# Kernel optimization log

Hardware: AMD Instinct MI355X
Metric: run time of the kernel (lower is better)

The kernel has to match this reference:

```python
import jax, jax.numpy as jnp
import numpy as np

B, C, T = 16, 768, 9
S = T * T * T            # 729 tokens
H = 8                    # heads
E = 3                    # experts
HID = C * 4              # expert hidden dim (mult=4)


def setup_inputs() -> dict:
    key = jax.random.key(0)
    ks = jax.random.split(key, 8)
    w = lambda k, sh: (jax.random.normal(k, sh, jnp.float32) * 0.02)
    return {
        "x": jax.random.normal(ks[0], (B, C, T, T, T), jnp.float32),
        "ln_gamma": jnp.ones((C, T, T, T), jnp.float32),
        "ln_beta": jnp.zeros((C, T, T, T), jnp.float32),
        "w_qkv": w(ks[1], (C, 3 * C)),
        "w_out": w(ks[2], (C, C)),
        "w_gate": w(ks[3], (C, E)),
        "b_gate": jnp.zeros((E,), jnp.float32),
        "w1": w(ks[4], (E, C, HID)),
        "b1": jnp.zeros((E, HID), jnp.float32),
        "w2": w(ks[5], (E, HID, C)),
        "b2": jnp.zeros((E, C), jnp.float32),
    }


def reference(x, ln_gamma, ln_beta, w_qkv, w_out, w_gate, b_gate, w1, b1, w2, b2):
    b = x.shape[0]
    # LayerNorm over (C, T, H, W) per batch element, affine params [C,T,T,T]
    mu = jnp.mean(x, axis=(1, 2, 3, 4), keepdims=True)
    var = jnp.var(x, axis=(1, 2, 3, 4), keepdims=True)
    xn = (x - mu) * jax.lax.rsqrt(var + 1e-5) * ln_gamma + ln_beta

    # ---- attention (NOTE: source applies no 1/sqrt(d) scaling) ----
    tok = xn.reshape(b, C, S).transpose(0, 2, 1)                 # [b,s,c]
    qkv = (tok @ w_qkv).reshape(b, S, 3, H, C // H)              # [b,s,3,h,d]
    q = qkv[:, :, 0].transpose(0, 2, 1, 3)                       # [b,h,s,d]
    k = qkv[:, :, 1].transpose(0, 2, 1, 3)
    v = qkv[:, :, 2].transpose(0, 2, 1, 3)
    attn = jax.nn.softmax(jnp.einsum('bhqd,bhkd->bhqk', q, k), axis=-1)
    ctx = jnp.einsum('bhqk,bhkd->bqhd', attn, v).reshape(b, S, C)
    attn_out = (ctx @ w_out).transpose(0, 2, 1).reshape(b, C, T, T, T)
    x2 = x + attn_out                                            # residual (dropout = eval identity)

    # ---- switch-MoE (top-1 gate, all experts computed densely then masked) ----
    tok2 = x2.reshape(b, C, S).transpose(0, 2, 1)                # [b,s,c]
    gate = jax.nn.softmax(tok2 @ w_gate + b_gate, axis=-1)       # [b,s,E]
    mask = jax.nn.one_hot(jnp.argmax(gate, axis=-1), E, dtype=gate.dtype)
    mg = gate * mask
    denom = jnp.sum(mg, axis=0, keepdims=True) + 1e-6            # sum over dim 0, per source
    gate_scores = mg / denom * b                                 # capacity = int(1.0 * b)

    hmid = jax.nn.gelu(jnp.einsum('bsc,ech->bseh', tok2, w1) + b1, approximate=False)
    eout = jnp.einsum('bseh,ehc->bsec', hmid, w2) + b2           # [b,s,E,c]
    moe = jnp.einsum('bse,bsec->bsc', gate_scores, eout)         # weighted mix over experts

    out = x2 + moe.transpose(0, 2, 1).reshape(b, C, T, T, T)
    return out
```

## Files before the change

### kernel.cpp

```cpp
#include <hip/hip_runtime.h>

typedef __bf16 bf16;
typedef __bf16 bf16x4_t __attribute__((ext_vector_type(4)));
typedef __bf16 bf16x8_t __attribute__((ext_vector_type(8)));
typedef float f32x4 __attribute__((ext_vector_type(4)));

#define DEVI __device__ __forceinline__

#define N_B   16
#define N_C   768
#define N_S   729
#define N_TOK 11664
#define TOKP  11776
#define N_H   8
#define N_D   96
#define N_HID 3072
#define MOE_TILES 94
#define GATE_BLOCKS 183

#define OFF_WQKVH 0ull
#define OFF_WQKVL 3538944ull
#define OFF_WOUTH 7077888ull
#define OFF_WOUTL 8257536ull
#define OFF_W1T   9437184ull
#define OFF_W2T   23592960ull
#define OFF_XTOK  37748736ull
#define OFF_R3    73924608ull
#define OFF_TOKH  OFF_R3
#define OFF_TOKL  (OFF_R3 + 18087936ull)
#define OFF_VTH   OFF_R3
#define OFF_VTL   (OFF_R3 + 18087936ull)
#define OFF_T2H   OFF_R3
#define OFF_QKH   110100480ull
#define OFF_QKL   146276352ull
#define OFF_VPH   182452224ull
#define OFF_VPL   200540160ull
#define OFF_CTXH  OFF_VPH
#define OFF_CTXL  OFF_VPL
#define OFF_HMID  OFF_QKH
#define OFF_X2    218628096ull
#define OFF_STATS 254803968ull
#define OFF_DENOM (OFF_STATS + 256ull)
#define OFF_SEL   (OFF_STATS + 16384ull)
#define OFF_PVAL  (OFF_SEL + 65536ull)
#define OFF_GSV   (OFF_PVAL + 65536ull)
#define OFF_PERM  (OFF_GSV + 65536ull)
#define OFF_CNT   (OFF_PERM + 65536ull)

DEVI f32x4 mfma16(bf16x8_t a, bf16x8_t b, f32x4 c) {
  return __builtin_amdgcn_mfma_f32_16x16x32_bf16(a, b, c, 0, 0, 0);
}
DEVI bf16 f2bf(float f) { return (bf16)f; }
DEVI float bf2f(bf16 h) { return (float)h; }
#define GLDS(gp, lp) __builtin_amdgcn_global_load_lds( \
    (__attribute__((address_space(1))) void*)(gp),     \
    (__attribute__((address_space(3))) void*)(lp), 16, 0, 0)

DEVI void xcd_swz(int& bx, int& by) {
  int gx = gridDim.x;
  int nwg = gx * gridDim.y;
  int lin = blockIdx.x + gx * blockIdx.y;
  int xcd = lin & 7, j = lin >> 3;
  int q = nwg >> 3, r = nwg & 7;
  int base = (xcd < r) ? xcd * (q + 1) : r * (q + 1) + (xcd - r) * q;
  int g = base + j;
  by = g / gx;
  bx = g - by * gx;
}

template<bool SPLIT>
__global__ void kxpose(const float* __restrict__ in, bf16* __restrict__ oh,
                       bf16* __restrict__ ol, int R, int Cc) {
  __shared__ float T[32][33];
  int c0 = blockIdx.x * 32, r0 = blockIdx.y * 32;
  int tx = threadIdx.x, ty = threadIdx.y;
#pragma unroll
  for (int i = 0; i < 4; i++)
    T[ty + i * 8][tx] = in[(size_t)(r0 + ty + i * 8) * Cc + c0 + tx];
  __syncthreads();
#pragma unroll
  for (int i = 0; i < 4; i++) {
    float v = T[tx][ty + i * 8];
    size_t o = (size_t)(c0 + ty + i * 8) * R + r0 + tx;
    bf16 hh = f2bf(v);
    oh[o] = hh;
    if constexpr (SPLIT) ol[o] = f2bf(v - bf2f(hh));
  }
}

__global__ __launch_bounds__(256) void ln_stats(const float* __restrict__ x,
                                                double* __restrict__ stats) {
  int b = blockIdx.x >> 7, ch = blockIdx.x & 127;
  const float* xb = x + (size_t)b * 559872;
  int start = ch * 4374;
  float s = 0.f, ss = 0.f;
  for (int i = start + threadIdx.x; i < start + 4374; i += 256) {
    float v = xb[i];
    s += v; ss += v * v;
  }
#pragma unroll
  for (int o = 32; o > 0; o >>= 1) { s += __shfl_down(s, o); ss += __shfl_down(ss, o); }
  __shared__ float rs[4], rss[4];
  int w = threadIdx.x >> 6;
  if ((threadIdx.x & 63) == 0) { rs[w] = s; rss[w] = ss; }
  __syncthreads();
  if (threadIdx.x == 0) {
    atomicAdd(&stats[b * 2 + 0], (double)(rs[0] + rs[1] + rs[2] + rs[3]));
    atomicAdd(&stats[b * 2 + 1], (double)(rss[0] + rss[1] + rss[2] + rss[3]));
  }
}

__global__ void ln_apply(const float* __restrict__ x, const float* __restrict__ g,
                         const float* __restrict__ be, const double* __restrict__ stats,
                         float* __restrict__ xtok, bf16* __restrict__ th, bf16* __restrict__ tl) {
  __shared__ float TN[32][33], TX[32][33];
  int b = blockIdx.z, c0 = blockIdx.y * 32, s0 = blockIdx.x * 32;
  double mu = stats[b * 2] * (1.0 / 559872.0);
  double var = stats[b * 2 + 1] * (1.0 / 559872.0) - mu * mu;
  float rstd = (float)(1.0 / sqrt(var + 1e-5));
  float muf = (float)mu;
  int tx = threadIdx.x, ty = threadIdx.y;
  size_t bo = (size_t)b * 559872;
#pragma unroll
  for (int i = 0; i < 4; i++) {
    int c = c0 + ty + i * 8, s = s0 + tx;
    float v = 0.f, xn = 0.f;
    if (s < N_S) {
      v = x[bo + (size_t)c * 729 + s];
      xn = (v - muf) * rstd * g[(size_t)c * 729 + s] + be[(size_t)c * 729 + s];
    }
    TX[ty + i * 8][tx] = v;
    TN[ty + i * 8][tx] = xn;
  }
  __syncthreads();
#pragma unroll
  for (int i = 0; i < 4; i++) {
    int s = s0 + ty + i * 8;
    if (s < N_S) {
      size_t tok = (size_t)b * 729 + s;
      int c = c0 + tx;
      float xv = TX[tx][ty + i * 8];
      float xn = TN[tx][ty + i * 8];
      xtok[tok * 768 + c] = xv;
      bf16 hh = f2bf(xn);
      th[tok * 768 + c] = hh;
      tl[tok * 768 + c] = f2bf(xn - bf2f(hh));
    }
  }
}

enum { EPI_HL = 0, EPI_ATTNOUT = 1 };

template<int EPI, bool SPLIT>
__global__ __launch_bounds__(256, 2)
void gemm_k(const bf16* __restrict__ Ah, const bf16* __restrict__ Al,
            const bf16* __restrict__ Bh, const bf16* __restrict__ Bl,
            int M, int N, int K,
            bf16* __restrict__ o0, bf16* __restrict__ o1, float* __restrict__ of,
            const float* __restrict__ fa) {
  __shared__ __align__(16) bf16 Ash[8192], Bsh[8192];
  __shared__ __align__(16) bf16 Asl[SPLIT ? 8192 : 8], Bsl[SPLIT ? 8192 : 8];
  const int t = threadIdx.x;
  const int lane = t & 63, w = t >> 6;
  const int wr = (w >> 1) << 6, wc = (w & 1) << 6;
  const int lr = lane & 15, lg = lane >> 4;
  int sbx, sby; xcd_swz(sbx, sby);
  const size_t arow = (size_t)sby * 128;
  const size_t brow = (size_t)sbx * 128;
  const int sr = t >> 3;
  const int sg = ((t & 7) ^ (sr & 7)) << 3;
  const bf16* pA = Ah + (arow + sr) * (size_t)K + sg;
  const bf16* pB = Bh + (brow + sr) * (size_t)K + sg;
  const bf16 *pAl = nullptr, *pBl = nullptr;
  if constexpr (SPLIT) {
    pAl = Al + (arow + sr) * (size_t)K + sg;
    pBl = Bl + (brow + sr) * (size_t)K + sg;
  }
  const size_t rstep = (size_t)K << 5;
  f32x4 acc[4][4] = {};
  for (int k0 = 0; k0 < K; k0 += 64) {
    __syncthreads();
#pragma unroll
    for (int c = 0; c < 4; c++) {
      GLDS(pA + c * rstep + k0, &Ash[c * 2048 + t * 8]);
      GLDS(pB + c * rstep + k0, &Bsh[c * 2048 + t * 8]);
      if constexpr (SPLIT) {
        GLDS(pAl + c * rstep + k0, &Asl[c * 2048 + t * 8]);
        GLDS(pBl + c * rstep + k0, &Bsl[c * 2048 + t * 8]);
      }
    }
    asm volatile("s_waitcnt vmcnt(0)" ::: "memory");
    __syncthreads();
#pragma unroll
    for (int kk = 0; kk < 2; kk++) {
      bf16x8_t af[4], bq[4], afl[4], bql[4];
#pragma unroll
      for (int m = 0; m < 4; m++) {
        int row = wr + m * 16 + lr;
        int off = row * 64 + ((((kk << 2) | lg) ^ (row & 7)) << 3);
        af[m] = *(const bf16x8_t*)&Ash[off];
        if constexpr (SPLIT) afl[m] = *(const bf16x8_t*)&Asl[off];
      }
#pragma unroll
      for (int n = 0; n < 4; n++) {
        int row = wc + n * 16 + lr;
        int off = row * 64 + ((((kk << 2) | lg) ^ (row & 7)) << 3);
        bq[n] = *(const bf16x8_t*)&Bsh[off];
        if constexpr (SPLIT) bql[n] = *(const bf16x8_t*)&Bsl[off];
      }
#pragma unroll
      for (int m = 0; m < 4; m++)
#pragma unroll
        for (int n = 0; n < 4; n++) {
          acc[m][n] = mfma16(af[m], bq[n], acc[m][n]);
          if constexpr (SPLIT) {
            acc[m][n] = mfma16(af[m], bql[n], acc[m][n]);
            acc[m][n] = mfma16(afl[m], bq[n], acc[m][n]);
          }
        }
    }
  }
#pragma unroll
  for (int m = 0; m < 4; m++) {
#pragma unroll
    for (int r = 0; r < 4; r++) {
      int gr = (int)arow + wr + m * 16 + lg * 4 + r;
      if (gr >= M) continue;
#pragma unroll
      for (int n = 0; n < 4; n++) {
        int gc = (int)brow + wc + n * 16 + lr;
        float v = acc[m][n][r];
        size_t oidx = (size_t)gr * N + gc;
        if constexpr (EPI == EPI_HL) {
          bf16 hh = f2bf(v);
          o0[oidx] = hh;
          o1[oidx] = f2bf(v - bf2f(hh));
        } else {
          float x2v = v + fa[(size_t)gr * 768 + gc];
          of[(size_t)gr * 768 + gc] = x2v;
          o0[(size_t)gr * 768 + gc] = f2bf(x2v);
        }
      }
    }
  }
}

__global__ __launch_bounds__(256, 3)
void gemm_moe1(const bf16* __restrict__ Ah, const bf16* __restrict__ W1T,
               const float* __restrict__ b1, const int* __restrict__ perm,
               const int* __restrict__ poff, bf16* __restrict__ hmid) {
  int sbx, sby; xcd_swz(sbx, sby);
  const int arow = sby * 128;
  if (arow >= poff[3]) return;
  const int e = (arow >= poff[1]) + (arow >= poff[2]);
  const bf16* Bh = W1T + (size_t)e * 3072 * 768;
  const float* bias = b1 + e * 3072;
  __shared__ __align__(16) bf16 Ash[8192], Bsh[8192];
  const int t = threadIdx.x;
  const int lane = t & 63, w = t >> 6;
  const int wr = (w >> 1) << 6, wc = (w & 1) << 6;
  const int lr = lane & 15, lg = lane >> 4;
  const size_t brow = (size_t)sbx * 128;
  const int sr = t >> 3;
  const int sg = ((t & 7) ^ (sr & 7)) << 3;
  int ip[4];
#pragma unroll
  for (int c = 0; c < 4; c++) {
    int ii = perm[arow + c * 32 + sr];
    ip[c] = (ii < 0) ? 0 : ii;
  }
  const bf16* pB = Bh + (brow + sr) * 768 + sg;
  const size_t rstep = 768ull << 5;
  f32x4 acc[4][4] = {};
  for (int k0 = 0; k0 < 768; k0 += 64) {
    __syncthreads();
#pragma unroll
    for (int c = 0; c < 4; c++) {
      GLDS(Ah + (size_t)ip[c] * 768 + sg + k0, &Ash[c * 2048 + t * 8]);
      GLDS(pB + c * rstep + k0, &Bsh[c * 2048 + t * 8]);
    }
    asm volatile("s_waitcnt vmcnt(0)" ::: "memory");
    __syncthreads();
#pragma unroll
    for (int kk = 0; kk < 2; kk++) {
      bf16x8_t af[4], bq[4];
#pragma unroll
      for (int m = 0; m < 4; m++) {
        int row = wr + m * 16 + lr;
        af[m] = *(const bf16x8_t*)&Ash[row * 64 + ((((kk << 2) | lg) ^ (row & 7)) << 3)];
      }
#pragma unroll
      for (int n = 0; n < 4; n++) {
        int row = wc + n * 16 + lr;
        bq[n] = *(const bf16x8_t*)&Bsh[row * 64 + ((((kk << 2) | lg) ^ (row & 7)) << 3)];
      }
#pragma unroll
      for (int m = 0; m < 4; m++)
#pragma unroll
        for (int n = 0; n < 4; n++)
          acc[m][n] = mfma16(af[m], bq[n], acc[m][n]);
    }
  }
#pragma unroll
  for (int m = 0; m < 4; m++)
#pragma unroll
    for (int r = 0; r < 4; r++) {
      int gr = arow + wr + m * 16 + lg * 4 + r;
#pragma unroll
      for (int n = 0; n < 4; n++) {
        int gc = (int)brow + wc + n * 16 + lr;
        float z = acc[m][n][r] + bias[gc];
        float gl = 0.5f * z * (1.f + erff(z * 0.7071067811865476f));
        hmid[(size_t)gr * 3072 + gc] = f2bf(gl);
      }
    }
}

__global__ __launch_bounds__(256, 3)
void gemm_moe2(const bf16* __restrict__ hmid, const bf16* __restrict__ W2T,
               const float* __restrict__ b2, const int* __restrict__ perm,
               const int* __restrict__ poff, const float* __restrict__ gsv,
               float* __restrict__ moe) {
  int sbx, sby; xcd_swz(sbx, sby);
  const int arow = sby * 128;
  if (arow >= poff[3]) return;
  const int e = (arow >= poff[1]) + (arow >= poff[2]);
  const bf16* Bh = W2T + (size_t)e * 768 * 3072;
  const float* bias = b2 + e * 768;
  __shared__ __align__(16) bf16 Ash[8192], Bsh[8192];
  const int t = threadIdx.x;
  const int lane = t & 63, w = t >> 6;
  const int wr = (w >> 1) << 6, wc = (w & 1) << 6;
  const int lr = lane & 15, lg = lane >> 4;
  const size_t brow = (size_t)sbx * 128;
  const int sr = t >> 3;
  const int sg = ((t & 7) ^ (sr & 7)) << 3;
  const bf16* pA = hmid + (size_t)(arow + sr) * 3072 + sg;
  const bf16* pB = Bh + (brow + sr) * 3072 + sg;
  const size_t rstep = 3072ull << 5;
  f32x4 acc[4][4] = {};
  for (int k0 = 0; k0 < 3072; k0 += 64) {
    __syncthreads();
#pragma unroll
    for (int c = 0; c < 4; c++) {
      GLDS(pA + c * rstep + k0, &Ash[c * 2048 + t * 8]);
      GLDS(pB + c * rstep + k0, &Bsh[c * 2048 + t * 8]);
    }
    asm volatile("s_waitcnt vmcnt(0)" ::: "memory");
    __syncthreads();
#pragma unroll
    for (int kk = 0; kk < 2; kk++) {
      bf16x8_t af[4], bq[4];
#pragma unroll
      for (int m = 0; m < 4; m++) {
        int row = wr + m * 16 + lr;
        af[m] = *(const bf16x8_t*)&Ash[row * 64 + ((((kk << 2) | lg) ^ (row & 7)) << 3)];
      }
#pragma unroll
      for (int n = 0; n < 4; n++) {
        int row = wc + n * 16 + lr;
        bq[n] = *(const bf16x8_t*)&Bsh[row * 64 + ((((kk << 2) | lg) ^ (row & 7)) << 3)];
      }
#pragma unroll
      for (int m = 0; m < 4; m++)
#pragma unroll
        for (int n = 0; n < 4; n++)
          acc[m][n] = mfma16(af[m], bq[n], acc[m][n]);
    }
  }
#pragma unroll
  for (int m = 0; m < 4; m++)
#pragma unroll
    for (int r = 0; r < 4; r++) {
      int gr = arow + wr + m * 16 + lg * 4 + r;
      int tok = perm[gr];
      if (tok < 0) continue;
      float gv = gsv[tok];
#pragma unroll
      for (int n = 0; n < 4; n++) {
        int gc = (int)brow + wc + n * 16 + lr;
        moe[(size_t)tok * 768 + gc] = (acc[m][n][r] + bias[gc]) * gv;
      }
    }
}

__global__ __launch_bounds__(256) void repack_v(const bf16* __restrict__ vph,
    const bf16* __restrict__ vpl, bf16* __restrict__ vth, bf16* __restrict__ vtl) {
  __shared__ bf16 Lh[96][40], Ll[96][40];
  int t = threadIdx.x;
  int bh = blockIdx.y, b = bh >> 3, h = bh & 7;
  int s0 = blockIdx.x * 32;
  for (int v = t; v < 384; v += 256) {
    int e0 = v * 8;
    int r = e0 / 96;
    int c = e0 - r * 96;
    size_t src = ((size_t)b * 729 + s0 + r) * 768 + h * 96 + c;
    bf16x8_t xh = *(const bf16x8_t*)&vph[src];
    bf16x8_t xl = *(const bf16x8_t*)&vpl[src];
    bool ok = (s0 + r) < N_S;
#pragma unroll
    for (int j = 0; j < 8; j++) {
      Lh[c + j][r] = ok ? xh[j] : f2bf(0.f);
      Ll[c + j][r] = ok ? xl[j] : f2bf(0.f);
    }
  }
  __syncthreads();
  for (int vv = t; vv < 768; vv += 256) {
    int e0 = vv * 4;
    int d = e0 >> 5, sl = e0 & 31;
    bf16x4_t ohv, olv;
#pragma unroll
    for (int j = 0; j < 4; j++) { ohv[j] = Lh[d][sl + j]; olv[j] = Ll[d][sl + j]; }
    size_t dst = (size_t)bh * (96ull * 736ull) + (size_t)d * 736 + s0 + sl;
    *(bf16x4_t*)&vth[dst] = ohv;
    *(bf16x4_t*)&vtl[dst] = olv;
  }
}

DEVI int pslot(int w, int s) { return ((s >> 9) << 11) + (w << 9) + (s & 511); }

__global__ __launch_bounds__(256, 3)
void attn(const bf16* __restrict__ qkh, const bf16* __restrict__ qkl,
          const bf16* __restrict__ vth, const bf16* __restrict__ vtl,
          bf16* __restrict__ ch, bf16* __restrict__ cl) {
  __shared__ bf16 Ksh[6144], Ksl[6144], Vsh[6144], Vsl[6144];
  const int t = threadIdx.x, lane = t & 63, w = t >> 6;
  const int lr = lane & 15, lg = lane >> 4;
  int sbx, sby; xcd_swz(sbx, sby);
  const int bh = sby, b = bh >> 3, h = bh & 7;
  const int q0 = sbx * 64;
  const size_t tokbase = (size_t)b * 729;
  const int qr = w * 16 + lr;
  const size_t qrow = (tokbase + q0 + qr) * 1536ull + (size_t)h * 96;
  bf16x8_t qh[3], ql[3];
#pragma unroll
  for (int ks = 0; ks < 3; ks++) {
    qh[ks] = *(const bf16x8_t*)&qkh[qrow + ks * 32 + lg * 8];
    ql[ks] = *(const bf16x8_t*)&qkl[qrow + ks * 32 + lg * 8];
  }

  auto loadK = [&](int kt) {
    const int kv0 = kt * 64;
#pragma unroll
    for (int chk = 0; chk < 3; chk++) {
      int kv = t >> 2, dg = t & 3;
      int sdg = dg ^ (kv & 3);
      size_t ksrc = (tokbase + kv0 + kv) * 1536ull + 768ull + (size_t)h * 96 + chk * 32 + (sdg << 3);
      int ldsoff = chk * 2048 + t * 8;
      GLDS(qkh + ksrc, &Ksh[ldsoff]);
      GLDS(qkl + ksrc, &Ksl[ldsoff]);
    }
  };
  auto loadV = [&](int kt) {
    const int kv0 = kt * 64;
#pragma unroll
    for (int chk = 0; chk < 3; chk++) {
      int ldsoff = chk * 2048 + t * 8;
      int d = ldsoff >> 6;
      int grp = (ldsoff >> 3) & 7;
      int sg = grp ^ (d & 7);
      size_t vsrc = (size_t)bh * (96ull * 736ull) + (size_t)d * 736 + kv0 + (sg << 3);
      GLDS(vth + vsrc, &Vsh[ldsoff]);
      GLDS(vtl + vsrc, &Vsl[ldsoff]);
    }
  };

  float mrow[4] = {-1e30f, -1e30f, -1e30f, -1e30f};
  float lpart[4] = {0.f, 0.f, 0.f, 0.f};
  f32x4 octx[6] = {};

  loadK(0);
  asm volatile("s_waitcnt vmcnt(0)" ::: "memory");
  __syncthreads();
  loadV(0);

  for (int kt = 0; kt < 12; kt++) {
    const int kv0 = kt * 64;
    f32x4 sc[4];
    __builtin_amdgcn_s_setprio(1);
#pragma unroll
    for (int cf = 0; cf < 4; cf++) {
      f32x4 a = {0.f, 0.f, 0.f, 0.f};
      int kvrow = cf * 16 + lr;
#pragma unroll
      for (int ks = 0; ks < 3; ks++) {
        int slot = ks * 2048 + kvrow * 32 + ((lg ^ (kvrow & 3)) << 3);
        bf16x8_t kh = *(const bf16x8_t*)&Ksh[slot];
        bf16x8_t kl = *(const bf16x8_t*)&Ksl[slot];
        a = mfma16(qh[ks], kh, a);
        a = mfma16(qh[ks], kl, a);
        a = mfma16(ql[ks], kh, a);
      }
      if (kv0 + kvrow >= N_S) { a[0] = -1e30f; a[1] = -1e30f; a[2] = -1e30f; a[3] = -1e30f; }
      sc[cf] = a;
    }
    __builtin_amdgcn_s_setprio(0);
    float lmax[4];
#pragma unroll
    for (int r = 0; r < 4; r++)
      lmax[r] = fmaxf(fmaxf(sc[0][r], sc[1][r]), fmaxf(sc[2][r], sc[3][r]));
    bool ok = (lmax[0] <= mrow[0] + 8.f) && (lmax[1] <= mrow[1] + 8.f) &&
              (lmax[2] <= mrow[2] + 8.f) && (lmax[3] <= mrow[3] + 8.f);
    if (!__all(ok)) {
      float escv[4];
#pragma unroll
      for (int r = 0; r < 4; r++) {
        float a = lmax[r];
#pragma unroll
        for (int o = 1; o < 16; o <<= 1) a = fmaxf(a, __shfl_xor(a, o));
        float mn = fmaxf(mrow[r], a);
        escv[r] = __expf(mrow[r] - mn);
        mrow[r] = mn;
        lpart[r] *= escv[r];
      }
#pragma unroll
      for (int df = 0; df < 6; df++)
#pragma unroll
        for (int r = 0; r < 4; r++) octx[df][r] *= escv[r];
    }
#pragma unroll
    for (int cf = 0; cf < 4; cf++)
#pragma unroll
      for (int r = 0; r < 4; r++) {
        float p = __expf(sc[cf][r] - mrow[r]);
        sc[cf][r] = p;
        lpart[r] += p;
      }
    asm volatile("s_waitcnt vmcnt(0)" ::: "memory");
    __syncthreads();
#pragma unroll
    for (int cf = 0; cf < 4; cf++)
#pragma unroll
      for (int r = 0; r < 4; r++) {
        int qloc = lg * 4 + r;
        int kvg = (cf << 1) | (lr >> 3);
        int xw = (qloc ^ (qloc >> 2)) & 7;
        int slot = qloc * 64 + (((kvg ^ xw) << 3) | (lr & 7));
        float p = sc[cf][r];
        bf16 hp = f2bf(p);
        int ps = pslot(w, slot);
        Ksh[ps] = hp;
        Ksl[ps] = f2bf(p - bf2f(hp));
      }
    asm volatile("s_waitcnt lgkmcnt(0)" ::: "memory");
    __builtin_amdgcn_sched_barrier(0);
    bf16x8_t pah[2], pal[2];
#pragma unroll
    for (int ks = 0; ks < 2; ks++) {
      int xr = (lr ^ (lr >> 2)) & 7;
      int slot = lr * 64 + ((((ks << 2) | lg) ^ xr) << 3);
      int ps = pslot(w, slot);
      pah[ks] = *(const bf16x8_t*)&Ksh[ps];
      pal[ks] = *(const bf16x8_t*)&Ksl[ps];
    }
    asm volatile("s_waitcnt lgkmcnt(0)" ::: "memory");
    __builtin_amdgcn_sched_barrier(0);
    if (kt < 11) loadK(kt + 1);
    __builtin_amdgcn_s_setprio(1);
#pragma unroll
    for (int df = 0; df < 6; df++) {
      int dd = df * 16 + lr;
#pragma unroll
      for (int ks = 0; ks < 2; ks++) {
        int slot = dd * 64 + ((((ks << 2) | lg) ^ (dd & 7)) << 3);
        bf16x8_t vh = *(const bf16x8_t*)&Vsh[slot];
        bf16x8_t vl = *(const bf16x8_t*)&Vsl[slot];
        octx[df] = mfma16(pah[ks], vh, octx[df]);
        octx[df] = mfma16(pah[ks], vl, octx[df]);
        octx[df] = mfma16(pal[ks], vh, octx[df]);
      }
    }
    __builtin_amdgcn_s_setprio(0);
    if (kt < 11) {
      asm volatile("s_waitcnt vmcnt(0)" ::: "memory");
      __syncthreads();
      loadV(kt + 1);
    }
  }
  float lrow[4];
#pragma unroll
  for (int r = 0; r < 4; r++) {
    float a = lpart[r];
#pragma unroll
    for (int o = 1; o < 16; o <<= 1) a += __shfl_xor(a, o);
    lrow[r] = a;
  }
#pragma unroll
  for (int r = 0; r < 4; r++) {
    int qloc = w * 16 + lg * 4 + r;
    if (q0 + qloc >= N_S) continue;
    size_t orow = (tokbase + q0 + qloc) * 768ull + (size_t)h * 96;
    float inv = 1.f / lrow[r];
#pragma unroll
    for (int df = 0; df < 6; df++) {
      float v = octx[df][r] * inv;
      bf16 hh = f2bf(v);
      ch[orow + df * 16 + lr] = hh;
      cl[orow + df * 16 + lr] = f2bf(v - bf2f(hh));
    }
  }
}

__global__ __launch_bounds__(256) void gate_k(const float* __restrict__ x2,
    const float* __restrict__ wg, const float* __restrict__ bg,
    int* __restrict__ sel, float* __restrict__ pval, float* __restrict__ denom,
    int* __restrict__ cnt) {
  int lane = threadIdx.x & 63, w = threadIdx.x >> 6;
  float wv[12][3];
#pragma unroll
  for (int j = 0; j < 12; j++) {
    int c = lane + j * 64;
    const float* wgc = wg + c * 3;
    wv[j][0] = wgc[0]; wv[j][1] = wgc[1]; wv[j][2] = wgc[2];
  }
  float bg0 = bg[0], bg1 = bg[1], bg2 = bg[2];
  int cloc0 = 0, cloc1 = 0, cloc2 = 0;
  int base_tok = (blockIdx.x * 4 + w) * 16;
  for (int it = 0; it < 16; it++) {
    int tok = base_tok + it;
    if (tok >= N_TOK) break;
    const float* row = x2 + (size_t)tok * 768;
    double a0 = 0, a1 = 0, a2 = 0;
#pragma unroll
    for (int j = 0; j < 12; j++) {
      float xv = row[lane + j * 64];
      a0 += (double)(xv * wv[j][0]);
      a1 += (double)(xv * wv[j][1]);
      a2 += (double)(xv * wv[j][2]);
    }
#pragma unroll
    for (int o = 32; o > 0; o >>= 1) {
      a0 += __shfl_down(a0, o);
      a1 += __shfl_down(a1, o);
      a2 += __shfl_down(a2, o);
    }
    if (lane == 0) {
      float g0 = (float)a0 + bg0, g1 = (float)a1 + bg1, g2 = (float)a2 + bg2;
      float mx = fmaxf(g0, fmaxf(g1, g2));
      float e0 = __expf(g0 - mx), e1 = __expf(g1 - mx), e2 = __expf(g2 - mx);
      float inv = 1.f / (e0 + e1 + e2);
      int am = 0; float pm = e0;
      if (e1 > pm) { pm = e1; am = 1; }
      if (e2 > pm) { pm = e2; am = 2; }
      float p = pm * inv;
      sel[tok] = am;
      pval[tok] = p;
      int s = tok - (tok / 729) * 729;
      atomicAdd(&denom[s * 3 + am], p);
      cloc0 += (am == 0); cloc1 += (am == 1); cloc2 += (am == 2);
    }
  }
  __shared__ int bc[3];
  if (threadIdx.x == 0) { bc[0] = 0; bc[1] = 0; bc[2] = 0; }
  __syncthreads();
  if (lane == 0) {
    if (cloc0) atomicAdd(&bc[0], cloc0);
    if (cloc1) atomicAdd(&bc[1], cloc1);
    if (cloc2) atomicAdd(&bc[2], cloc2);
  }
  __syncthreads();
  if (threadIdx.x < 3 && bc[threadIdx.x]) atomicAdd(&cnt[threadIdx.x], bc[threadIdx.x]);
}

__global__ void moe_scan(const int* __restrict__ cnt, int* __restrict__ poff) {
  int p1 = (cnt[0] + 127) & ~127;
  int p2 = p1 + ((cnt[1] + 127) & ~127);
  int p3 = p2 + ((cnt[2] + 127) & ~127);
  poff[0] = 0; poff[1] = p1; poff[2] = p2; poff[3] = p3;
}

__global__ __launch_bounds__(256) void moe_scatter(const int* __restrict__ sel,
                            const float* __restrict__ pval,
                            const float* __restrict__ denom, const int* __restrict__ poff,
                            int* __restrict__ cur, int* __restrict__ perm,
                            float* __restrict__ gsv) {
  int tok = blockIdx.x * 256 + threadIdx.x;
  int lane = threadIdx.x & 63, w = threadIdx.x >> 6;
  bool valid = tok < N_TOK;
  int e = valid ? sel[tok] : -1;
  if (valid) {
    int s = tok - (tok / 729) * 729;
    gsv[tok] = pval[tok] * 16.f / (denom[s * 3 + e] + 1e-6f);
  }
  unsigned long long m0 = __ballot(e == 0);
  unsigned long long m1 = __ballot(e == 1);
  unsigned long long m2 = __ballot(e == 2);
  __shared__ int wcnt[4][3], wbase[4][3];
  if (lane == 0) {
    wcnt[w][0] = __popcll(m0);
    wcnt[w][1] = __popcll(m1);
    wcnt[w][2] = __popcll(m2);
  }
  __syncthreads();
  if (threadIdx.x < 3) {
    int x = threadIdx.x;
    int c0 = wcnt[0][x], c1 = wcnt[1][x], c2 = wcnt[2][x], c3 = wcnt[3][x];
    int base = atomicAdd(&cur[x], c0 + c1 + c2 + c3);
    wbase[0][x] = base;
    wbase[1][x] = base + c0;
    wbase[2][x] = base + c0 + c1;
    wbase[3][x] = base + c0 + c1 + c2;
  }
  __syncthreads();
  if (valid) {
    unsigned long long lt = (lane == 0) ? 0ull : ((~0ull) >> (64 - lane));
    unsigned long long me = (e == 0) ? m0 : (e == 1) ? m1 : m2;
    int pos = wbase[w][e] + __popcll(me & lt);
    perm[poff[e] + pos] = tok;
  }
}

__global__ void final_k(const float* __restrict__ x2, const float* __restrict__ moe,
                        float* __restrict__ out) {
  __shared__ float L[32][33];
  int b = blockIdx.z, c0 = blockIdx.y * 32, s0 = blockIdx.x * 32;
  int tx = threadIdx.x, ty = threadIdx.y;
#pragma unroll
  for (int i = 0; i < 4; i++) {
    int s = s0 + ty + i * 8;
    float v = 0.f;
    if (s < N_S) {
      size_t tok = (size_t)b * 729 + s;
      v = x2[tok * 768 + c0 + tx] + moe[tok * 768 + c0 + tx];
    }
    L[ty + i * 8][tx] = v;
  }
  __syncthreads();
#pragma unroll
  for (int i = 0; i < 4; i++) {
    int s = s0 + tx;
    int c = c0 + ty + i * 8;
    if (s < N_S) out[((size_t)b * 768 + c) * 729 + s] = L[tx][ty + i * 8];
  }
}

extern "C" void kernel_launch(void* const* d_in, const int* in_sizes, int n_in,
                              void* d_out, int out_size, void* d_ws, size_t ws_size,
                              hipStream_t stream) {
  (void)in_sizes; (void)n_in; (void)out_size; (void)ws_size;
  const float* x     = (const float*)d_in[0];
  const float* lng   = (const float*)d_in[1];
  const float* lnb   = (const float*)d_in[2];
  const float* wqkv  = (const float*)d_in[3];
  const float* wout  = (const float*)d_in[4];
  const float* wgate = (const float*)d_in[5];
  const float* bgate = (const float*)d_in[6];
  const float* w1    = (const float*)d_in[7];
  const float* b1    = (const float*)d_in[8];
  const float* w2    = (const float*)d_in[9];
  const float* b2    = (const float*)d_in[10];
  float* out = (float*)d_out;
  char* ws = (char*)d_ws;

  bf16* WQKVH = (bf16*)(ws + OFF_WQKVH);
  bf16* WQKVL = (bf16*)(ws + OFF_WQKVL);
  bf16* WOUTH = (bf16*)(ws + OFF_WOUTH);
  bf16* WOUTL = (bf16*)(ws + OFF_WOUTL);
  bf16* W1T   = (bf16*)(ws + OFF_W1T);
  bf16* W2T   = (bf16*)(ws + OFF_W2T);
  float* XTOK = (float*)(ws + OFF_XTOK);
  float* MOE  = (float*)(ws + OFF_XTOK);
  bf16* TOKH  = (bf16*)(ws + OFF_TOKH);
  bf16* TOKL  = (bf16*)(ws + OFF_TOKL);
  bf16* VTH   = (bf16*)(ws + OFF_VTH);
  bf16* VTL   = (bf16*)(ws + OFF_VTL);
  bf16* T2H   = (bf16*)(ws + OFF_T2H);
  bf16* QKH   = (bf16*)(ws + OFF_QKH);
  bf16* QKL   = (bf16*)(ws + OFF_QKL);
  bf16* VPH   = (bf16*)(ws + OFF_VPH);
  bf16* VPL   = (bf16*)(ws + OFF_VPL);
  bf16* CTXH  = (bf16*)(ws + OFF_CTXH);
  bf16* CTXL  = (bf16*)(ws + OFF_CTXL);
  bf16* HMID  = (bf16*)(ws + OFF_HMID);
  float* X2   = (float*)(ws + OFF_X2);
  double* STATS = (double*)(ws + OFF_STATS);
  float* DENOM  = (float*)(ws + OFF_DENOM);
  int*   SEL    = (int*)(ws + OFF_SEL);
  float* PVAL   = (float*)(ws + OFF_PVAL);
  float* GSV    = (float*)(ws + OFF_GSV);
  int*   PERM   = (int*)(ws + OFF_PERM);
  int*   CNT    = (int*)(ws + OFF_CNT);
  int*   POFF   = CNT + 4;
  int*   CUR    = CNT + 8;

  hipMemsetAsync(ws + OFF_STATS, 0, 16384, stream);
  hipMemsetAsync(ws + OFF_CNT, 0, 64, stream);
  hipMemsetAsync(ws + OFF_PERM, 0xFF, MOE_TILES * 128 * 4, stream);

  dim3 tb(32, 8);
  kxpose<true><<<dim3(72, 24), tb, 0, stream>>>(wqkv, WQKVH, WQKVL, 768, 2304);
  kxpose<true><<<dim3(24, 24), tb, 0, stream>>>(wout, WOUTH, WOUTL, 768, 768);
  for (int e = 0; e < 3; e++) {
    kxpose<false><<<dim3(96, 24), tb, 0, stream>>>(w1 + (size_t)e * 768 * 3072,
        W1T + (size_t)e * 3072 * 768, nullptr, 768, 3072);
    kxpose<false><<<dim3(24, 96), tb, 0, stream>>>(w2 + (size_t)e * 3072 * 768,
        W2T + (size_t)e * 768 * 3072, nullptr, 3072, 768);
  }
  ln_stats<<<2048, 256, 0, stream>>>(x, STATS);
  ln_apply<<<dim3(23, 24, 16), tb, 0, stream>>>(x, lng, lnb, STATS, XTOK, TOKH, TOKL);
  gemm_k<EPI_HL, true><<<dim3(12, 92), 256, 0, stream>>>(
      TOKH, TOKL, WQKVH, WQKVL, N_TOK, 1536, 768, QKH, QKL, nullptr, nullptr);
  gemm_k<EPI_HL, true><<<dim3(6, 92), 256, 0, stream>>>(
      TOKH, TOKL, WQKVH + 1536 * 768, WQKVL + 1536 * 768, N_TOK, 768, 768,
      VPH, VPL, nullptr, nullptr);
  repack_v<<<dim3(23, 128), 256, 0, stream>>>(VPH, VPL, VTH, VTL);
  attn<<<dim3(12, 128), 256, 0, stream>>>(QKH, QKL, VTH, VTL, CTXH, CTXL);
  gemm_k<EPI_ATTNOUT, true><<<dim3(6, 92), 256, 0, stream>>>(
      CTXH, CTXL, WOUTH, WOUTL, N_TOK, 768, 768, T2H, nullptr, X2, XTOK);
  gate_k<<<GATE_BLOCKS, 256, 0, stream>>>(X2, wgate, bgate, SEL, PVAL, DENOM, CNT);
  moe_scan<<<1, 1, 0, stream>>>(CNT, POFF);
  moe_scatter<<<46, 256, 0, stream>>>(SEL, PVAL, DENOM, POFF, CUR, PERM, GSV);
  gemm_moe1<<<dim3(24, MOE_TILES), 256, 0, stream>>>(T2H, W1T, b1, PERM, POFF, HMID);
  gemm_moe2<<<dim3(6, MOE_TILES), 256, 0, stream>>>(HMID, W2T, b2, PERM, POFF, GSV, MOE);
  final_k<<<dim3(23, 24, 16), tb, 0, stream>>>(X2, MOE, out);
}
```

Measured before the change: 672.3 us.

## Widen attention blocks to 128 queries and give P its own LDS buffer

```diff
diff --git a/kernel.cpp b/kernel.cpp
--- a/kernel.cpp
+++ b/kernel.cpp
@@ -417,18 +417,17 @@
   }
 }
 
-DEVI int pslot(int w, int s) { return ((s >> 9) << 11) + (w << 9) + (s & 511); }
-
-__global__ __launch_bounds__(256, 3)
+__global__ __launch_bounds__(512, 4)
 void attn(const bf16* __restrict__ qkh, const bf16* __restrict__ qkl,
           const bf16* __restrict__ vth, const bf16* __restrict__ vtl,
           bf16* __restrict__ ch, bf16* __restrict__ cl) {
   __shared__ bf16 Ksh[6144], Ksl[6144], Vsh[6144], Vsl[6144];
+  __shared__ bf16 Ph[8][1024], Pl[8][1024];
   const int t = threadIdx.x, lane = t & 63, w = t >> 6;
   const int lr = lane & 15, lg = lane >> 4;
   int sbx, sby; xcd_swz(sbx, sby);
   const int bh = sby, b = bh >> 3, h = bh & 7;
-  const int q0 = sbx * 64;
+  const int q0 = sbx * 128;
   const size_t tokbase = (size_t)b * 729;
   const int qr = w * 16 + lr;
   const size_t qrow = (tokbase + q0 + qr) * 1536ull + (size_t)h * 96;
@@ -442,26 +441,33 @@
   auto loadK = [&](int kt) {
     const int kv0 = kt * 64;
 #pragma unroll
-    for (int chk = 0; chk < 3; chk++) {
-      int kv = t >> 2, dg = t & 3;
-      int sdg = dg ^ (kv & 3);
-      size_t ksrc = (tokbase + kv0 + kv) * 1536ull + 768ull + (size_t)h * 96 + chk * 32 + (sdg << 3);
-      int ldsoff = chk * 2048 + t * 8;
-      GLDS(qkh + ksrc, &Ksh[ldsoff]);
-      GLDS(qkl + ksrc, &Ksl[ldsoff]);
+    for (int pass = 0; pass < 2; pass++) {
+      int g = pass * 512 + t;
+      if (g < 768) {
+        int chunk = g >> 8, tt = g & 255;
+        int kv = tt >> 2, dg = tt & 3;
+        int sdg = dg ^ (kv & 3);
+        size_t ksrc = (tokbase + kv0 + kv) * 1536ull + 768ull + (size_t)h * 96 + chunk * 32 + (sdg << 3);
+        int ldsoff = g * 8;
+        GLDS(qkh + ksrc, &Ksh[ldsoff]);
+        GLDS(qkl + ksrc, &Ksl[ldsoff]);
+      }
     }
   };
   auto loadV = [&](int kt) {
     const int kv0 = kt * 64;
 #pragma unroll
-    for (int chk = 0; chk < 3; chk++) {
-      int ldsoff = chk * 2048 + t * 8;
-      int d = ldsoff >> 6;
-      int grp = (ldsoff >> 3) & 7;
-      int sg = grp ^ (d & 7);
-      size_t vsrc = (size_t)bh * (96ull * 736ull) + (size_t)d * 736 + kv0 + (sg << 3);
-      GLDS(vth + vsrc, &Vsh[ldsoff]);
-      GLDS(vtl + vsrc, &Vsl[ldsoff]);
+    for (int pass = 0; pass < 2; pass++) {
+      int g = pass * 512 + t;
+      if (g < 768) {
+        int ldsoff = g * 8;
+        int d = g >> 3;
+        int grp = g & 7;
+        int sg = grp ^ (d & 7);
+        size_t vsrc = (size_t)bh * (96ull * 736ull) + (size_t)d * 736 + kv0 + (sg << 3);
+        GLDS(vth + vsrc, &Vsh[ldsoff]);
+        GLDS(vtl + vsrc, &Vsl[ldsoff]);
+      }
     }
   };
 
@@ -528,6 +534,7 @@
       }
     asm volatile("s_waitcnt vmcnt(0)" ::: "memory");
     __syncthreads();
+    if (kt < 11) loadK(kt + 1);
 #pragma unroll
     for (int cf = 0; cf < 4; cf++)
 #pragma unroll
@@ -538,9 +545,8 @@
         int slot = qloc * 64 + (((kvg ^ xw) << 3) | (lr & 7));
         float p = sc[cf][r];
         bf16 hp = f2bf(p);
-        int ps = pslot(w, slot);
-        Ksh[ps] = hp;
-        Ksl[ps] = f2bf(p - bf2f(hp));
+        Ph[w][slot] = hp;
+        Pl[w][slot] = f2bf(p - bf2f(hp));
       }
     asm volatile("s_waitcnt lgkmcnt(0)" ::: "memory");
     __builtin_amdgcn_sched_barrier(0);
@@ -549,13 +555,11 @@
     for (int ks = 0; ks < 2; ks++) {
       int xr = (lr ^ (lr >> 2)) & 7;
       int slot = lr * 64 + ((((ks << 2) | lg) ^ xr) << 3);
-      int ps = pslot(w, slot);
-      pah[ks] = *(const bf16x8_t*)&Ksh[ps];
-      pal[ks] = *(const bf16x8_t*)&Ksl[ps];
+      pah[ks] = *(const bf16x8_t*)&Ph[w][slot];
+      pal[ks] = *(const bf16x8_t*)&Pl[w][slot];
     }
     asm volatile("s_waitcnt lgkmcnt(0)" ::: "memory");
     __builtin_amdgcn_sched_barrier(0);
-    if (kt < 11) loadK(kt + 1);
     __builtin_amdgcn_s_setprio(1);
 #pragma unroll
     for (int df = 0; df < 6; df++) {
@@ -804,7 +808,7 @@
       TOKH, TOKL, WQKVH + 1536 * 768, WQKVL + 1536 * 768, N_TOK, 768, 768,
       VPH, VPL, nullptr, nullptr);
   repack_v<<<dim3(23, 128), 256, 0, stream>>>(VPH, VPL, VTH, VTL);
-  attn<<<dim3(12, 128), 256, 0, stream>>>(QKH, QKL, VTH, VTL, CTXH, CTXL);
+  attn<<<dim3(6, 128), 512, 0, stream>>>(QKH, QKL, VTH, VTL, CTXH, CTXL);
   gemm_k<EPI_ATTNOUT, true><<<dim3(6, 92), 256, 0, stream>>>(
       CTXH, CTXL, WOUTH, WOUTL, N_TOK, 768, 768, T2H, nullptr, X2, XTOK);
   gate_k<<<GATE_BLOCKS, 256, 0, stream>>>(X2, wgate, bgate, SEL, PVAL, DENOM, CNT);
```

New measurement: 865.8 us. +28.8%, slower.
